# Optimization experiments

Hardware: AMD Instinct MI355X
Metric: run time of the kernel (lower is better)

The kernel has to match this reference:

```python
import jax, jax.numpy as jnp
import numpy as np
import math

HEADS = 8

def setup_inputs() -> dict:
    key = jax.random.key(0)
    k1, k2 = jax.random.split(key)
    B, C, H, W = 8, 512, 32, 32
    x = jax.random.normal(k1, (B, C, H, W), dtype=jnp.float32)
    # weight-norm 1x1 conv params: v ~ N(0, 0.05), g initialized to ||v|| (torch weight_norm default)
    proj_v = jax.random.normal(k2, (3 * C, C), dtype=jnp.float32) * 0.05
    proj_g = jnp.linalg.norm(proj_v, axis=1)
    proj_b = jnp.zeros((3 * C,), dtype=jnp.float32)
    return {"x": x, "proj_v": proj_v, "proj_g": proj_g, "proj_b": proj_b}

def reference(x, proj_v, proj_g, proj_b):
    B, C, H, W = x.shape
    heads = HEADS
    dim = C // heads
    N = H * W
    # weight-normalized 1x1 conv: w = g * v / ||v|| per output channel
    w = proj_g[:, None] * proj_v / jnp.linalg.norm(proj_v, axis=1, keepdims=True)
    c = jnp.einsum('oc,bchw->bohw', w, x) + proj_b[None, :, None, None]
    c = c.reshape(B, 3, heads, dim, N)
    q, k, v = c[:, 0], c[:, 1], c[:, 2]  # each (B, heads, dim, N)
    scale = 1.0 / math.sqrt(dim)
    attn = jnp.einsum('bhdq,bhdk->bhqk', q, k) * scale  # (B, heads, N, N)
    attn = jax.nn.softmax(attn, axis=-1)
    out = jnp.einsum('bhdk,bhqk->bhdq', v, attn)  # (B, heads, dim, N)
    return x + out.reshape(B, C, H, W)
```

## Files before the change

### kernel.cpp

```cpp
#include <hip/hip_runtime.h>

typedef _Float16 f16;
typedef _Float16 f16x4 __attribute__((ext_vector_type(4)));
typedef _Float16 f16x8 __attribute__((ext_vector_type(8)));
typedef float f32x4 __attribute__((ext_vector_type(4)));

__device__ inline f32x4 mfma16(f16x8 a, f16x8 b, f32x4 c) {
    return __builtin_amdgcn_mfma_f32_16x16x32_f16(a, b, c, 0, 0, 0);
}

__device__ inline void st8(f16* p, f16x8 v) {
    *(f16x4*)p = __builtin_shufflevector(v, v, 0, 1, 2, 3);
    *(f16x4*)(p + 4) = __builtin_shufflevector(v, v, 4, 5, 6, 7);
}
__device__ inline f16x8 ld8(const f16* p) {
    f16x4 lo = *(const f16x4*)p;
    f16x4 hi = *(const f16x4*)(p + 4);
    return __builtin_shufflevector(lo, hi, 0, 1, 2, 3, 4, 5, 6, 7);
}

__global__ __launch_bounds__(256) void compute_w_k(const float* __restrict__ pv,
                                                   const float* __restrict__ pg,
                                                   f16* __restrict__ w) {
    int o = blockIdx.x;
    const float* row = pv + (size_t)o * 512;
    float s = 0.f;
    for (int c = threadIdx.x; c < 512; c += 256) { float t = row[c]; s += t * t; }
    for (int off = 32; off; off >>= 1) s += __shfl_down(s, off, 64);
    __shared__ float red[4];
    int lane = threadIdx.x & 63, wid = threadIdx.x >> 6;
    if (lane == 0) red[wid] = s;
    __syncthreads();
    float tot = red[0] + red[1] + red[2] + red[3];
    float scale = pg[o] * rsqrtf(tot);
    for (int c = threadIdx.x; c < 512; c += 256)
        w[(size_t)o * 512 + c] = (f16)(row[c] * scale);
}

__global__ __launch_bounds__(256) void transpose_x_k(const float* __restrict__ x,
                                                     f16* __restrict__ xT) {
    __shared__ float t[32][33];
    int b = blockIdx.z, n0 = blockIdx.x * 32, c0 = blockIdx.y * 32;
    int tx = threadIdx.x, ty = threadIdx.y;
    const float* xb = x + (size_t)b * 512 * 1024;
    for (int i = 0; i < 4; i++)
        t[ty + 8 * i][tx] = xb[(size_t)(c0 + ty + 8 * i) * 1024 + n0 + tx];
    __syncthreads();
    f16* xTb = xT + (size_t)b * 1024 * 512;
    for (int i = 0; i < 4; i++)
        xTb[(size_t)(n0 + ty + 8 * i) * 512 + c0 + tx] = (f16)t[tx][ty + 8 * i];
}

#define GLDA 40
__global__ __launch_bounds__(256) void qkv_gemm_k(const f16* __restrict__ w,
                                                  const f16* __restrict__ xT,
                                                  const float* __restrict__ pb,
                                                  f16* __restrict__ qk,
                                                  f16* __restrict__ v) {
    __shared__ f16 lA[128 * GLDA];
    __shared__ f16 lB[128 * GLDA];
    int b = blockIdx.z;
    int oBase = blockIdx.y * 128;
    int nBase = blockIdx.x * 128;
    const f16* xb = xT + (size_t)b * 1024 * 512;
    int tid = threadIdx.x;
    int lane = tid & 63, warp = tid >> 6;
    int wy = warp >> 1, wx = warp & 1;
    int quad = lane >> 4, l15 = lane & 15;

    f32x4 acc[4][4] = {};

    for (int k0 = 0; k0 < 512; k0 += 32) {
        __syncthreads();
        for (int c = tid; c < 512; c += 256) {
            int row = c >> 2, col = (c & 3) * 8;
            *(f16x8*)&lA[row * GLDA + col] =
                *(const f16x8*)&w[(size_t)(oBase + row) * 512 + k0 + col];
            *(f16x8*)&lB[row * GLDA + col] =
                *(const f16x8*)&xb[(size_t)(nBase + row) * 512 + k0 + col];
        }
        __syncthreads();
        f16x8 af[4], bf[4];
        for (int mi = 0; mi < 4; mi++)
            af[mi] = *(f16x8*)&lA[(wy * 64 + mi * 16 + l15) * GLDA + quad * 8];
        for (int ni = 0; ni < 4; ni++)
            bf[ni] = *(f16x8*)&lB[(wx * 64 + ni * 16 + l15) * GLDA + quad * 8];
        for (int mi = 0; mi < 4; mi++)
            for (int ni = 0; ni < 4; ni++)
                acc[mi][ni] = mfma16(af[mi], bf[ni], acc[mi][ni]);
    }

    for (int mi = 0; mi < 4; mi++) {
        int oRow = oBase + wy * 64 + mi * 16 + quad * 4;
        for (int ni = 0; ni < 4; ni++) {
            int n = nBase + wx * 64 + ni * 16 + l15;
            for (int reg = 0; reg < 4; reg++) {
                int oo = oRow + reg;
                float val = acc[mi][ni][reg] + pb[oo];
                int sel = oo >> 9, h = (oo >> 6) & 7, d = oo & 63;
                if (sel == 0) val *= 0.125f;
                if (sel < 2)
                    qk[((((size_t)b * 2 + sel) * 8 + h) * 1024 + n) * 64 + d] = (f16)val;
                else
                    v[(((size_t)b * 8 + h) * 64 + d) * 1024 + n] = (f16)val;
            }
        }
    }
}

#define ALDK 68
__global__ __launch_bounds__(256) void attn_k(const f16* __restrict__ qk,
                                              const f16* __restrict__ vg,
                                              const float* __restrict__ x,
                                              float* __restrict__ out) {
    __shared__ __align__(16) f16 smem[3 * 64 * ALDK];
    f16* lK = smem;
    f16* lV = smem + 64 * ALDK;
    f16* lPb = smem + 2 * 64 * ALDK;
    float* OT = (float*)smem;

    int bh = blockIdx.y;
    int b = bh >> 3, h = bh & 7;
    int qBase = blockIdx.x * 64;
    int tid = threadIdx.x, lane = tid & 63, warp = tid >> 6;
    int quad = lane >> 4, l15 = lane & 15;

    const f16* qbase = qk + (((size_t)b * 2 + 0) * 8 + h) * 1024 * 64;
    const f16* kbase = qk + (((size_t)b * 2 + 1) * 8 + h) * 1024 * 64;
    const f16* vbase = vg + ((size_t)b * 8 + h) * 64 * 1024;
    f16* lP = lPb + warp * 16 * ALDK;

    int q0 = qBase + warp * 16;
    f16x8 aq[2];
    for (int kh = 0; kh < 2; kh++)
        aq[kh] = *(const f16x8*)&qbase[(size_t)(q0 + l15) * 64 + kh * 32 + quad * 8];

    int sr0 = tid >> 3, sc0 = (tid & 7) * 8;
    int sr1 = (tid + 256) >> 3, sc1 = sc0;

    f16x8 rK[2], rV[2];
    rK[0] = *(const f16x8*)&kbase[(size_t)sr0 * 64 + sc0];
    rK[1] = *(const f16x8*)&kbase[(size_t)sr1 * 64 + sc1];
    rV[0] = *(const f16x8*)&vbase[(size_t)sr0 * 1024 + sc0];
    rV[1] = *(const f16x8*)&vbase[(size_t)sr1 * 1024 + sc1];

    f32x4 accO[4] = {};
    float m_cur = -1e30f, l_cur = 0.f;

    for (int kt = 0; kt < 16; kt++) {
        __syncthreads();
        st8(&lK[sr0 * ALDK + sc0], rK[0]);
        st8(&lK[sr1 * ALDK + sc1], rK[1]);
        st8(&lV[sr0 * ALDK + sc0], rV[0]);
        st8(&lV[sr1 * ALDK + sc1], rV[1]);
        __syncthreads();
        if (kt < 15) {
            const f16* kb = kbase + (size_t)(kt + 1) * 64 * 64;
            rK[0] = *(const f16x8*)&kb[(size_t)sr0 * 64 + sc0];
            rK[1] = *(const f16x8*)&kb[(size_t)sr1 * 64 + sc1];
            rV[0] = *(const f16x8*)&vbase[(size_t)sr0 * 1024 + (kt + 1) * 64 + sc0];
            rV[1] = *(const f16x8*)&vbase[(size_t)sr1 * 1024 + (kt + 1) * 64 + sc1];
        }

        f32x4 st[4] = {};
        for (int mt = 0; mt < 4; mt++)
            for (int kh = 0; kh < 2; kh++) {
                f16x8 ak = ld8(&lK[(mt * 16 + l15) * ALDK + kh * 32 + quad * 8]);
                st[mt] = mfma16(ak, aq[kh], st[mt]);
            }

        float mx = m_cur;
        for (int mt = 0; mt < 4; mt++)
            for (int r = 0; r < 4; r++) mx = fmaxf(mx, st[mt][r]);
        mx = fmaxf(mx, __shfl_xor(mx, 16, 64));
        mx = fmaxf(mx, __shfl_xor(mx, 32, 64));
        float alpha = __expf(m_cur - mx);
        m_cur = mx;
        float rs = 0.f;
        for (int mt = 0; mt < 4; mt++) {
            f16x4 pk;
            for (int r = 0; r < 4; r++) {
                float p = __expf(st[mt][r] - mx);
                rs += p;
                pk[r] = (f16)p;
            }
            *(f16x4*)&lP[l15 * ALDK + mt * 16 + quad * 4] = pk;
        }
        rs += __shfl_xor(rs, 16, 64);
        rs += __shfl_xor(rs, 32, 64);
        l_cur = l_cur * alpha + rs;
        for (int dt = 0; dt < 4; dt++) accO[dt] *= alpha;

        for (int kh = 0; kh < 2; kh++) {
            f16x8 bp = ld8(&lP[l15 * ALDK + kh * 32 + quad * 8]);
            for (int dt = 0; dt < 4; dt++) {
                f16x8 av = ld8(&lV[(dt * 16 + l15) * ALDK + kh * 32 + quad * 8]);
                accO[dt] = mfma16(av, bp, accO[dt]);
            }
        }
    }

    __syncthreads();
    float rl = 1.0f / l_cur;
    for (int dt = 0; dt < 4; dt++)
        for (int r = 0; r < 4; r++)
            OT[(dt * 16 + quad * 4 + r) * ALDK + warp * 16 + l15] = accO[dt][r] * rl;
    __syncthreads();
    for (int i = 0; i < 4; i++) {
        int cid = tid + 256 * i;
        int d = cid >> 4, qi = (cid & 15) * 4;
        float4 o4 = *(float4*)&OT[d * ALDK + qi];
        size_t gi = ((size_t)b * 512 + h * 64 + d) * 1024 + qBase + qi;
        float4 xv = *(const float4*)&x[gi];
        o4.x += xv.x; o4.y += xv.y; o4.z += xv.z; o4.w += xv.w;
        *(float4*)&out[gi] = o4;
    }
}

extern "C" void kernel_launch(void* const* d_in, const int* in_sizes, int n_in,
                              void* d_out, int out_size, void* d_ws, size_t ws_size,
                              hipStream_t stream) {
    (void)in_sizes; (void)n_in; (void)out_size; (void)ws_size;
    const float* x  = (const float*)d_in[0];
    const float* pv = (const float*)d_in[1];
    const float* pg = (const float*)d_in[2];
    const float* pb = (const float*)d_in[3];
    float* out = (float*)d_out;

    char* ws = (char*)d_ws;
    f16* w   = (f16*)(ws);
    f16* xT  = (f16*)(ws + 1572864);
    f16* qk  = (f16*)(ws + 1572864 + 8388608);
    f16* v   = (f16*)(ws + 1572864 + 8388608 + 16777216);

    hipLaunchKernelGGL(compute_w_k,  dim3(1536),      dim3(256),   0, stream, pv, pg, w);
    hipLaunchKernelGGL(transpose_x_k, dim3(32, 16, 8), dim3(32, 8), 0, stream, x, xT);
    hipLaunchKernelGGL(qkv_gemm_k,   dim3(8, 12, 8),  dim3(256),   0, stream, w, xT, pb, qk, v);
    hipLaunchKernelGGL(attn_k,       dim3(16, 64),    dim3(256),   0, stream, qk, v, x, out);
}
```

Baseline: 153.1 us.

## Use direct global-to-LDS loads with XOR swizzle in QKV GEMM, widen attention LDS accesses

The QKV projection GEMM now uses global_load_lds to copy tiles straight into shared memory without staging through registers. It doubles the K tile to 64 and applies an XOR swizzle so fragment reads avoid bank conflicts without padding. The attention kernel's LDS stride becomes 72 so that 16-byte vector loads and stores stay aligned, replacing the split 8-byte accesses. The softmax max and sum reductions are split into independent chains to expose more ILP. The risks are the correctness of the swizzle and of the direct-to-LDS load addressing, and the larger LDS footprint per block.

```diff
diff --git a/kernel.cpp b/kernel.cpp
--- a/kernel.cpp
+++ b/kernel.cpp
@@ -4,19 +4,16 @@
 typedef _Float16 f16x4 __attribute__((ext_vector_type(4)));
 typedef _Float16 f16x8 __attribute__((ext_vector_type(8)));
 typedef float f32x4 __attribute__((ext_vector_type(4)));
+typedef unsigned int u32;
 
 __device__ inline f32x4 mfma16(f16x8 a, f16x8 b, f32x4 c) {
     return __builtin_amdgcn_mfma_f32_16x16x32_f16(a, b, c, 0, 0, 0);
 }
 
-__device__ inline void st8(f16* p, f16x8 v) {
-    *(f16x4*)p = __builtin_shufflevector(v, v, 0, 1, 2, 3);
-    *(f16x4*)(p + 4) = __builtin_shufflevector(v, v, 4, 5, 6, 7);
-}
-__device__ inline f16x8 ld8(const f16* p) {
-    f16x4 lo = *(const f16x4*)p;
-    f16x4 hi = *(const f16x4*)(p + 4);
-    return __builtin_shufflevector(lo, hi, 0, 1, 2, 3, 4, 5, 6, 7);
+__device__ inline void gl2lds16(const f16* g, f16* l) {
+    __builtin_amdgcn_global_load_lds(
+        (const __attribute__((address_space(1))) u32*)g,
+        (__attribute__((address_space(3))) u32*)l, 16, 0, 0);
 }
 
 __global__ __launch_bounds__(256) void compute_w_k(const float* __restrict__ pv,
@@ -51,43 +48,54 @@
         xTb[(size_t)(n0 + ty + 8 * i) * 512 + c0 + tx] = (f16)t[tx][ty + 8 * i];
 }
 
-#define GLDA 40
 __global__ __launch_bounds__(256) void qkv_gemm_k(const f16* __restrict__ w,
                                                   const f16* __restrict__ xT,
                                                   const float* __restrict__ pb,
                                                   f16* __restrict__ qk,
                                                   f16* __restrict__ v) {
-    __shared__ f16 lA[128 * GLDA];
-    __shared__ f16 lB[128 * GLDA];
+    __shared__ f16 lA[128 * 64];
+    __shared__ f16 lB[128 * 64];
     int b = blockIdx.z;
     int oBase = blockIdx.y * 128;
     int nBase = blockIdx.x * 128;
     const f16* xb = xT + (size_t)b * 1024 * 512;
-    int tid = threadIdx.x;
-    int lane = tid & 63, warp = tid >> 6;
+    int tid = threadIdx.x, lane = tid & 63, warp = tid >> 6;
     int wy = warp >> 1, wx = warp & 1;
     int quad = lane >> 4, l15 = lane & 15;
 
+    int srow = lane >> 3;
+    int schunk = (lane & 7) ^ srow;
+    const f16* aSrc[4]; const f16* bSrc[4]; f16* aDst[4]; f16* bDst[4];
+    for (int j = 0; j < 4; j++) {
+        int rb = (warp * 4 + j) * 8;
+        aSrc[j] = w  + (size_t)(oBase + rb + srow) * 512 + schunk * 8;
+        bSrc[j] = xb + (size_t)(nBase + rb + srow) * 512 + schunk * 8;
+        aDst[j] = lA + rb * 64;
+        bDst[j] = lB + rb * 64;
+    }
+    int ph0 = (quad ^ (l15 & 7)) * 8;
+    int ph1 = ((4 + quad) ^ (l15 & 7)) * 8;
+
     f32x4 acc[4][4] = {};
 
-    for (int k0 = 0; k0 < 512; k0 += 32) {
-        __syncthreads();
-        for (int c = tid; c < 512; c += 256) {
-            int row = c >> 2, col = (c & 3) * 8;
-            *(f16x8*)&lA[row * GLDA + col] =
-                *(const f16x8*)&w[(size_t)(oBase + row) * 512 + k0 + col];
-            *(f16x8*)&lB[row * GLDA + col] =
-                *(const f16x8*)&xb[(size_t)(nBase + row) * 512 + k0 + col];
-        }
-        __syncthreads();
-        f16x8 af[4], bf[4];
-        for (int mi = 0; mi < 4; mi++)
-            af[mi] = *(f16x8*)&lA[(wy * 64 + mi * 16 + l15) * GLDA + quad * 8];
-        for (int ni = 0; ni < 4; ni++)
-            bf[ni] = *(f16x8*)&lB[(wx * 64 + ni * 16 + l15) * GLDA + quad * 8];
-        for (int mi = 0; mi < 4; mi++)
+    for (int k0 = 0; k0 < 512; k0 += 64) {
+        __syncthreads();
+        for (int j = 0; j < 4; j++) {
+            gl2lds16(aSrc[j] + k0, aDst[j]);
+            gl2lds16(bSrc[j] + k0, bDst[j]);
+        }
+        __syncthreads();
+        for (int kh = 0; kh < 2; kh++) {
+            int ph = kh ? ph1 : ph0;
+            f16x8 af[4], bf[4];
+            for (int mi = 0; mi < 4; mi++)
+                af[mi] = *(f16x8*)&lA[(wy * 64 + mi * 16 + l15) * 64 + ph];
             for (int ni = 0; ni < 4; ni++)
-                acc[mi][ni] = mfma16(af[mi], bf[ni], acc[mi][ni]);
+                bf[ni] = *(f16x8*)&lB[(wx * 64 + ni * 16 + l15) * 64 + ph];
+            for (int mi = 0; mi < 4; mi++)
+                for (int ni = 0; ni < 4; ni++)
+                    acc[mi][ni] = mfma16(af[mi], bf[ni], acc[mi][ni]);
+        }
     }
 
     for (int mi = 0; mi < 4; mi++) {
@@ -108,7 +116,7 @@
     }
 }
 
-#define ALDK 68
+#define ALDK 72
 __global__ __launch_bounds__(256) void attn_k(const f16* __restrict__ qk,
                                               const f16* __restrict__ vg,
                                               const float* __restrict__ x,
@@ -149,10 +157,10 @@
 
     for (int kt = 0; kt < 16; kt++) {
         __syncthreads();
-        st8(&lK[sr0 * ALDK + sc0], rK[0]);
-        st8(&lK[sr1 * ALDK + sc1], rK[1]);
-        st8(&lV[sr0 * ALDK + sc0], rV[0]);
-        st8(&lV[sr1 * ALDK + sc1], rV[1]);
+        *(f16x8*)&lK[sr0 * ALDK + sc0] = rK[0];
+        *(f16x8*)&lK[sr1 * ALDK + sc1] = rK[1];
+        *(f16x8*)&lV[sr0 * ALDK + sc0] = rV[0];
+        *(f16x8*)&lV[sr1 * ALDK + sc1] = rV[1];
         __syncthreads();
         if (kt < 15) {
             const f16* kb = kbase + (size_t)(kt + 1) * 64 * 64;
@@ -165,36 +173,41 @@
         f32x4 st[4] = {};
         for (int mt = 0; mt < 4; mt++)
             for (int kh = 0; kh < 2; kh++) {
-                f16x8 ak = ld8(&lK[(mt * 16 + l15) * ALDK + kh * 32 + quad * 8]);
+                f16x8 ak = *(f16x8*)&lK[(mt * 16 + l15) * ALDK + kh * 32 + quad * 8];
                 st[mt] = mfma16(ak, aq[kh], st[mt]);
             }
 
-        float mx = m_cur;
-        for (int mt = 0; mt < 4; mt++)
-            for (int r = 0; r < 4; r++) mx = fmaxf(mx, st[mt][r]);
+        float t0 = fmaxf(fmaxf(st[0][0], st[0][1]), fmaxf(st[0][2], st[0][3]));
+        float t1 = fmaxf(fmaxf(st[1][0], st[1][1]), fmaxf(st[1][2], st[1][3]));
+        float t2 = fmaxf(fmaxf(st[2][0], st[2][1]), fmaxf(st[2][2], st[2][3]));
+        float t3 = fmaxf(fmaxf(st[3][0], st[3][1]), fmaxf(st[3][2], st[3][3]));
+        float mx = fmaxf(fmaxf(t0, t1), fmaxf(t2, t3));
+        mx = fmaxf(mx, m_cur);
         mx = fmaxf(mx, __shfl_xor(mx, 16, 64));
         mx = fmaxf(mx, __shfl_xor(mx, 32, 64));
         float alpha = __expf(m_cur - mx);
         m_cur = mx;
-        float rs = 0.f;
+        float rs0 = 0.f, rs1 = 0.f, rs2 = 0.f, rs3 = 0.f;
         for (int mt = 0; mt < 4; mt++) {
             f16x4 pk;
-            for (int r = 0; r < 4; r++) {
-                float p = __expf(st[mt][r] - mx);
-                rs += p;
-                pk[r] = (f16)p;
-            }
+            float p0 = __expf(st[mt][0] - mx);
+            float p1 = __expf(st[mt][1] - mx);
+            float p2 = __expf(st[mt][2] - mx);
+            float p3 = __expf(st[mt][3] - mx);
+            rs0 += p0; rs1 += p1; rs2 += p2; rs3 += p3;
+            pk[0] = (f16)p0; pk[1] = (f16)p1; pk[2] = (f16)p2; pk[3] = (f16)p3;
             *(f16x4*)&lP[l15 * ALDK + mt * 16 + quad * 4] = pk;
         }
+        float rs = (rs0 + rs1) + (rs2 + rs3);
         rs += __shfl_xor(rs, 16, 64);
         rs += __shfl_xor(rs, 32, 64);
         l_cur = l_cur * alpha + rs;
         for (int dt = 0; dt < 4; dt++) accO[dt] *= alpha;
 
         for (int kh = 0; kh < 2; kh++) {
-            f16x8 bp = ld8(&lP[l15 * ALDK + kh * 32 + quad * 8]);
+            f16x8 bp = *(f16x8*)&lP[l15 * ALDK + kh * 32 + quad * 8];
             for (int dt = 0; dt < 4; dt++) {
-                f16x8 av = ld8(&lV[(dt * 16 + l15) * ALDK + kh * 32 + quad * 8]);
+                f16x8 av = *(f16x8*)&lV[(dt * 16 + l15) * ALDK + kh * 32 + quad * 8];
                 accO[dt] = mfma16(av, bp, accO[dt]);
             }
         }
```

New measurement: 158.5 us. 3.5% more time.
